# Performance work log

Measured on AMD Instinct MI355X. Metric: run time of the kernel, lower is better.

## Reference

```python
import jax, jax.numpy as jnp
import numpy as np
from jax import lax

B, C, XH, XW, KH, KW = 32, 128, 96, 96, 3, 3
BN_EPS = 1e-5


def setup_inputs() -> dict:
    key = jax.random.key(0)
    k1, k2, k3 = jax.random.split(key, 3)
    x = jax.random.normal(k1, (B, C, XH, XW), dtype=jnp.float32)
    k = jax.random.normal(k2, (B, C, KH, KW), dtype=jnp.float32)
    pw_weight = jax.random.normal(k3, (C, C), dtype=jnp.float32) * (1.0 / np.sqrt(C))
    bn_gamma = jnp.ones((C,), dtype=jnp.float32)
    bn_beta = jnp.zeros((C,), dtype=jnp.float32)
    bn_mean = jnp.zeros((C,), dtype=jnp.float32)
    bn_var = jnp.ones((C,), dtype=jnp.float32)
    return {"x": x, "k": k, "pw_weight": pw_weight, "bn_gamma": bn_gamma,
            "bn_beta": bn_beta, "bn_mean": bn_mean, "bn_var": bn_var}


def _depthwise_one(xi, ki):
    # xi: [C, XH, XW], ki: [C, KH, KW] -> per-sample depthwise conv, padding=KH//2
    pad = KH // 2
    out = lax.conv_general_dilated(
        xi[None],                 # [1, C, XH, XW]
        ki[:, None],              # [C, 1, KH, KW]  (OIHW with groups=C)
        window_strides=(1, 1),
        padding=((pad, pad), (pad, pad)),
        feature_group_count=C,
        dimension_numbers=("NCHW", "OIHW", "NCHW"),
    )
    return out[0]


def reference(x, k, pw_weight, bn_gamma, bn_beta, bn_mean, bn_var):
    # Per-sample dynamic depthwise conv, batched via vmap (replaces the Python loop)
    x_new = jax.vmap(_depthwise_one)(x, k)          # [B, C, XH, XW]
    # 1x1 pointwise conv (no bias)
    y = jnp.einsum("bchw,oc->bohw", x_new, pw_weight)
    # BatchNorm (inference form with running stats) + ReLU
    inv = bn_gamma * lax.rsqrt(bn_var + BN_EPS)
    y = y * inv[None, :, None, None] + (bn_beta - bn_mean * inv)[None, :, None, None]
    return jax.nn.relu(y)
```

## Files before the change

### kernel.cpp

```cpp
#include <hip/hip_runtime.h>
#include <hip/hip_bf16.h>

#define BB 32
#define CC 128
#define HH 96
#define WW 96
#define BN_EPS 1e-5f

typedef __attribute__((ext_vector_type(8))) short bf16x8_t;
typedef __attribute__((ext_vector_type(4))) float f32x4_t;
typedef __attribute__((ext_vector_type(4), aligned(4))) float f32x4u_t;
typedef __attribute__((ext_vector_type(2))) unsigned int u32x2_t;
typedef __attribute__((ext_vector_type(4))) unsigned int u32x4_t;

__global__ __launch_bounds__(256)
void prep_kernel(const float* __restrict__ pw,
                 const float* __restrict__ g, const float* __restrict__ b,
                 const float* __restrict__ m, const float* __restrict__ v,
                 unsigned short* __restrict__ wper,
                 float* __restrict__ inv, float* __restrict__ bias)
{
    int t = blockIdx.x * 256 + threadIdx.x;
    if (t < CC * CC) {
        int o = t >> 7, cidx = t & 127;
        int kc = cidx >> 5, r = cidx & 31, gg = r >> 3, j = r & 7;
        int c = kc * 32 + gg * 4 + (j & 3) + 16 * (j >> 2);
        __hip_bfloat16 h = __float2bfloat16(pw[o * CC + c]);
        wper[o * CC + cidx] = *reinterpret_cast<unsigned short*>(&h);
    }
    if (t < CC) {
        float iv = g[t] * rsqrtf(v[t] + BN_EPS);
        inv[t] = iv;
        bias[t] = b[t] - m[t] * iv;
    }
}

__global__ __launch_bounds__(256, 6)
void dw_kernel(const float* __restrict__ x, const float* __restrict__ kk,
               unsigned short* __restrict__ xn)
{
    const unsigned wg  = blockIdx.x;
    const unsigned bid = (wg & 7u) * 2304u + (wg >> 3);
    const int u = (int)bid * 256 + threadIdx.x;
    const int lane = threadIdx.x & 63;
    const int woct = u % 12;
    int t1 = u / 12;
    const int h = t1 % HH;
    int t2 = t1 / HH;
    const int cs = t2 & 127;
    const int b  = t2 >> 7;

    const int kc = cs >> 5, rr = cs & 31, gg = rr >> 3, jj = rr & 7;
    const int c = kc * 32 + gg * 4 + (jj & 3) + 16 * (jj >> 2);

    const int w0 = woct * 8;
    const bool l_edge = (woct == 0);
    const bool r_edge = (woct == 11);

    const float* plane = x + (size_t)(b * CC + c) * (HH * WW);

    float kw[9];
    {
        const float* kp = kk + (size_t)(b * CC + c) * 9;
        f32x4u_t q0 = *(const f32x4u_t*)(kp);
        f32x4u_t q1 = *(const f32x4u_t*)(kp + 4);
        kw[0]=q0.x; kw[1]=q0.y; kw[2]=q0.z; kw[3]=q0.w;
        kw[4]=q1.x; kw[5]=q1.y; kw[6]=q1.z; kw[7]=q1.w;
        kw[8]=kp[8];
    }

    float r0[10], r1[10], r2[10];
    auto load_row = [&](int row, float* o) {
        const bool valid = (row >= 0) && (row < HH);
        const int rrow = row < 0 ? 0 : (row >= HH ? HH - 1 : row);
        const float* rp = plane + rrow * WW + w0;
        f32x4_t M0 = *(const f32x4_t*)rp;
        f32x4_t M1 = *(const f32x4_t*)(rp + 4);
        float vl = __shfl_up(M1.w, 1);
        float vr = __shfl_down(M0.x, 1);
        if (lane == 0  && !l_edge) vl = rp[-1];
        if (lane == 63 && !r_edge) vr = rp[8];
        o[0] = (valid && !l_edge) ? vl : 0.f;
        o[1] = valid ? M0.x : 0.f;
        o[2] = valid ? M0.y : 0.f;
        o[3] = valid ? M0.z : 0.f;
        o[4] = valid ? M0.w : 0.f;
        o[5] = valid ? M1.x : 0.f;
        o[6] = valid ? M1.y : 0.f;
        o[7] = valid ? M1.z : 0.f;
        o[8] = valid ? M1.w : 0.f;
        o[9] = (valid && !r_edge) ? vr : 0.f;
    };

    load_row(h - 1, r0);
    load_row(h,     r1);
    load_row(h + 1, r2);

    unsigned pkw[4];
    #pragma unroll
    for (int i = 0; i < 4; ++i) {
        float s0 = 0.f, s1 = 0.f;
        #pragma unroll
        for (int t = 0; t < 3; ++t) {
            s0 = fmaf(r0[2 * i + t],     kw[t],     s0);
            s0 = fmaf(r1[2 * i + t],     kw[3 + t], s0);
            s0 = fmaf(r2[2 * i + t],     kw[6 + t], s0);
            s1 = fmaf(r0[2 * i + 1 + t], kw[t],     s1);
            s1 = fmaf(r1[2 * i + 1 + t], kw[3 + t], s1);
            s1 = fmaf(r2[2 * i + 1 + t], kw[6 + t], s1);
        }
        __hip_bfloat16 h0b = __float2bfloat16(s0);
        __hip_bfloat16 h1b = __float2bfloat16(s1);
        pkw[i] = (unsigned)*reinterpret_cast<unsigned short*>(&h0b)
               | ((unsigned)*reinterpret_cast<unsigned short*>(&h1b) << 16);
    }
    u32x4_t pk;
    pk.x = pkw[0]; pk.y = pkw[1]; pk.z = pkw[2]; pk.w = pkw[3];
    unsigned short* dst = xn + ((size_t)(b * CC + cs) * (HH * WW) + (size_t)h * WW + w0);
    *reinterpret_cast<u32x4_t*>(dst) = pk;
}

__global__ __launch_bounds__(256, 3)
void pw_kernel(const unsigned short* __restrict__ xn,
               const unsigned short* __restrict__ wper,
               const float* __restrict__ invp, const float* __restrict__ biasp,
               float* __restrict__ out)
{
    __shared__ __align__(16) unsigned char xnb[128 * 256];
    const int tid = threadIdx.x;

    const unsigned wg  = blockIdx.x;
    const unsigned nid = (wg & 7u) * 96u + (wg >> 3);
    const int tw  = nid % 6u;
    const int thg = (nid / 6u) % 4u;
    const int b   = nid / 24u;
    const int w0  = tw * 16;

    const int lane   = tid & 63;
    const int wv     = tid >> 6;
    const int lo     = lane & 15;
    const int hi     = lane >> 4;
    const int o_base = wv * 32;

    bf16x8_t wfrag[2][4];
    #pragma unroll
    for (int t2 = 0; t2 < 2; ++t2)
        #pragma unroll
        for (int kc = 0; kc < 4; ++kc)
            wfrag[t2][kc] = *reinterpret_cast<const bf16x8_t*>(
                wper + (size_t)(o_base + t2 * 16 + lo) * CC + kc * 32 + hi * 8);

    float iv2[2], bs2[2];
    #pragma unroll
    for (int t2 = 0; t2 < 2; ++t2) {
        iv2[t2] = invp[o_base + t2 * 16 + lo];
        bs2[t2] = biasp[o_base + t2 * 16 + lo];
    }

    const int cs4 = tid >> 3;
    const int py  = tid & 7;
    const unsigned short* src_base =
        xn + (size_t)(b * CC + cs4 * 4) * (HH * WW) + (size_t)py * WW + w0;

    unsigned dLA[4][4], dRA[4][4], dLB[4][4], dRB[4][4];

    auto LOADREGS = [&](int t, unsigned (*dL)[4], unsigned (*dR)[4]) {
        const unsigned short* s0 = src_base + (size_t)((thg * 3 + t) * 8) * WW;
        #pragma unroll
        for (int q = 0; q < 4; ++q) {
            const unsigned short* src = s0 + (size_t)q * (HH * WW);
            u32x4_t L = *(const u32x4_t*)src;
            u32x4_t R = *(const u32x4_t*)(src + 8);
            dL[q][0]=L.x; dL[q][1]=L.y; dL[q][2]=L.z; dL[q][3]=L.w;
            dR[q][0]=R.x; dR[q][1]=R.y; dR[q][2]=R.z; dR[q][3]=R.w;
        }
    };

    auto WRITE_LDS = [&](unsigned (*dL)[4], unsigned (*dR)[4]) {
        #pragma unroll
        for (int o8 = 0; o8 < 2; ++o8) {
            #pragma unroll
            for (int j = 0; j < 4; ++j) {
                const unsigned d0 = o8 ? dR[0][j] : dL[0][j];
                const unsigned d1 = o8 ? dR[1][j] : dL[1][j];
                const unsigned d2 = o8 ? dR[2][j] : dL[2][j];
                const unsigned d3 = o8 ? dR[3][j] : dL[3][j];
                u32x2_t we, wo;
                we.x = __builtin_amdgcn_perm(d1, d0, 0x05040100u);
                we.y = __builtin_amdgcn_perm(d3, d2, 0x05040100u);
                wo.x = __builtin_amdgcn_perm(d1, d0, 0x07060302u);
                wo.y = __builtin_amdgcn_perm(d3, d2, 0x07060302u);
                const int pe = py * 16 + o8 * 8 + 2 * j;
                const int po = pe + 1;
                *reinterpret_cast<u32x2_t*>(&xnb[(unsigned)pe * 256 +
                    (((unsigned)cs4 * 8) ^ (((unsigned)pe & 7u) << 4))]) = we;
                *reinterpret_cast<u32x2_t*>(&xnb[(unsigned)po * 256 +
                    (((unsigned)cs4 * 8) ^ (((unsigned)po & 7u) << 4))]) = wo;
            }
        }
    };

    auto COMPUTE = [&](int t) {
        const int h0 = (thg * 3 + t) * 8;
        f32x4_t acc[8][2];
        #pragma unroll
        for (int pt = 0; pt < 8; ++pt) {
            acc[pt][0] = (f32x4_t){0.f, 0.f, 0.f, 0.f};
            acc[pt][1] = (f32x4_t){0.f, 0.f, 0.f, 0.f};
        }
        #pragma unroll
        for (int pt = 0; pt < 8; ++pt) {
            const unsigned rowbase = (unsigned)(pt * 16 + lo) * 256;
            const unsigned sw = (unsigned)((lo & 7) << 4);
            #pragma unroll
            for (int kc = 0; kc < 4; ++kc) {
                bf16x8_t xfrag = *reinterpret_cast<const bf16x8_t*>(
                    &xnb[rowbase + (((unsigned)(kc * 64 + hi * 16)) ^ sw)]);
                acc[pt][0] = __builtin_amdgcn_mfma_f32_16x16x32_bf16(
                    xfrag, wfrag[0][kc], acc[pt][0], 0, 0, 0);
                acc[pt][1] = __builtin_amdgcn_mfma_f32_16x16x32_bf16(
                    xfrag, wfrag[1][kc], acc[pt][1], 0, 0, 0);
            }
        }
        #pragma unroll
        for (int pt = 0; pt < 8; ++pt) {
            const int hrow = h0 + pt;
            #pragma unroll
            for (int t2 = 0; t2 < 2; ++t2) {
                const int o = o_base + t2 * 16 + lo;
                f32x4_t vv;
                #pragma unroll
                for (int r = 0; r < 4; ++r)
                    vv[r] = fmaxf(fmaf(acc[pt][t2][r], iv2[t2], bs2[t2]), 0.f);
                __builtin_nontemporal_store(vv, reinterpret_cast<f32x4_t*>(
                    out + ((size_t)(b * CC + o) * HH + hrow) * WW + w0 + hi * 4));
            }
        }
    };

    LOADREGS(0, dLA, dRA);
    WRITE_LDS(dLA, dRA);
    LOADREGS(1, dLB, dRB);
    __syncthreads();
    COMPUTE(0);
    __syncthreads();
    WRITE_LDS(dLB, dRB);
    LOADREGS(2, dLA, dRA);
    __syncthreads();
    COMPUTE(1);
    __syncthreads();
    WRITE_LDS(dLA, dRA);
    __syncthreads();
    COMPUTE(2);
}

__global__ __launch_bounds__(256, 3)
void fused_main(const float* __restrict__ x, const float* __restrict__ kk,
                const unsigned short* __restrict__ wper,
                const float* __restrict__ invp, const float* __restrict__ biasp,
                float* __restrict__ out)
{
    __shared__ __align__(16) unsigned char xnb[128 * 256];
    const int tid = threadIdx.x;
    const unsigned wg  = blockIdx.x;
    const unsigned nid = (wg & 7u) * 288u + (wg >> 3);
    const int bx = nid % 6u;
    const int by = (nid / 6u) % 12u;
    const int bb = nid / 72u;
    const int w0 = bx * 16;
    const int h0 = by * 8;
    {
        const int wq = tid & 3;
        const int cp = tid >> 2;
        const int s  = cp << 1;
        const int kc = s >> 5, rr = s & 31, gg = rr >> 3, jj = rr & 7;
        const int cA = kc * 32 + gg * 4 + (jj & 3) + 16 * (jj >> 2);
        const int gw = w0 + wq * 4;
        const bool l_edge = (gw == 0);
        const bool r_edge = (gw + 4 >= WW);
        const float* planeA = x + (size_t)(bb * CC + cA) * (HH * WW);
        float kwA[9], kwB[9];
        {
            const float* kp = kk + (size_t)(bb * CC + cA) * 9;
            f32x4u_t q0 = *(const f32x4u_t*)(kp + 0);
            f32x4u_t q1 = *(const f32x4u_t*)(kp + 4);
            f32x4u_t q2 = *(const f32x4u_t*)(kp + 8);
            f32x4u_t q3 = *(const f32x4u_t*)(kp + 12);
            float     e16 = kp[16], e17 = kp[17];
            kwA[0]=q0.x; kwA[1]=q0.y; kwA[2]=q0.z; kwA[3]=q0.w;
            kwA[4]=q1.x; kwA[5]=q1.y; kwA[6]=q1.z; kwA[7]=q1.w;
            kwA[8]=q2.x;
            kwB[0]=q2.y; kwB[1]=q2.z; kwB[2]=q2.w;
            kwB[3]=q3.x; kwB[4]=q3.y; kwB[5]=q3.z; kwB[6]=q3.w;
            kwB[7]=e16;  kwB[8]=e17;
        }
        float xd[2][10][6];
        #pragma unroll
        for (int q = 0; q < 2; ++q) {
            const float* plane = planeA + q * (HH * WW);
            #pragma unroll
            for (int r = 0; r < 10; ++r) {
                const int row = h0 - 1 + r;
                const bool valid = (row >= 0) && (row < HH);
                const int rrow = row < 0 ? 0 : (row >= HH ? HH - 1 : row);
                const float* rp = plane + rrow * WW + gw;
                f32x4_t M = *(const f32x4_t*)rp;
                float vl = rp[l_edge ? 0 : -1];
                float vr = rp[r_edge ? 3 : 4];
                xd[q][r][0] = (valid && !l_edge) ? vl : 0.f;
                xd[q][r][1] = valid ? M.x : 0.f;
                xd[q][r][2] = valid ? M.y : 0.f;
                xd[q][r][3] = valid ? M.z : 0.f;
                xd[q][r][4] = valid ? M.w : 0.f;
                xd[q][r][5] = (valid && !r_edge) ? vr : 0.f;
            }
        }
        #pragma unroll
        for (int py = 0; py < 8; ++py) {
            #pragma unroll
            for (int i = 0; i < 4; ++i) {
                float sA = 0.f, sB = 0.f;
                #pragma unroll
                for (int t = 0; t < 3; ++t) {
                    sA = fmaf(xd[0][py + 0][i + t], kwA[t],     sA);
                    sA = fmaf(xd[0][py + 1][i + t], kwA[3 + t], sA);
                    sA = fmaf(xd[0][py + 2][i + t], kwA[6 + t], sA);
                    sB = fmaf(xd[1][py + 0][i + t], kwB[t],     sB);
                    sB = fmaf(xd[1][py + 1][i + t], kwB[3 + t], sB);
                    sB = fmaf(xd[1][py + 2][i + t], kwB[6 + t], sB);
                }
                __hip_bfloat16 hA = __float2bfloat16(sA);
                __hip_bfloat16 hB = __float2bfloat16(sB);
                unsigned pk = (unsigned)*reinterpret_cast<unsigned short*>(&hA)
                            | ((unsigned)*reinterpret_cast<unsigned short*>(&hB) << 16);
                const int p = py * 16 + wq * 4 + i;
                const unsigned boff = ((unsigned)(cp << 2)) ^ (((unsigned)p & 7u) << 4);
                *reinterpret_cast<unsigned*>(&xnb[(unsigned)p * 256 + boff]) = pk;
            }
        }
    }
    __syncthreads();
    {
        const int lane   = tid & 63;
        const int wv     = tid >> 6;
        const int lo     = lane & 15;
        const int hi     = lane >> 4;
        const int o_base = wv * 32;
        bf16x8_t afrag[2][4];
        #pragma unroll
        for (int t2 = 0; t2 < 2; ++t2)
            #pragma unroll
            for (int kc = 0; kc < 4; ++kc)
                afrag[t2][kc] = *reinterpret_cast<const bf16x8_t*>(
                    wper + (size_t)(o_base + t2 * 16 + lo) * CC + kc * 32 + hi * 8);
        f32x4_t acc[8][2];
        #pragma unroll
        for (int pt = 0; pt < 8; ++pt) {
            acc[pt][0] = (f32x4_t){0.f, 0.f, 0.f, 0.f};
            acc[pt][1] = (f32x4_t){0.f, 0.f, 0.f, 0.f};
        }
        #pragma unroll
        for (int pt = 0; pt < 8; ++pt) {
            const unsigned rowbase = (unsigned)(pt * 16 + lo) * 256;
            const unsigned sw = (unsigned)((lo & 7) << 4);
            #pragma unroll
            for (int kc = 0; kc < 4; ++kc) {
                bf16x8_t bfrag = *reinterpret_cast<const bf16x8_t*>(
                    &xnb[rowbase + (((unsigned)(kc * 64 + hi * 16)) ^ sw)]);
                acc[pt][0] = __builtin_amdgcn_mfma_f32_16x16x32_bf16(
                    afrag[0][kc], bfrag, acc[pt][0], 0, 0, 0);
                acc[pt][1] = __builtin_amdgcn_mfma_f32_16x16x32_bf16(
                    afrag[1][kc], bfrag, acc[pt][1], 0, 0, 0);
            }
        }
        float iv[2][4], bs[2][4];
        #pragma unroll
        for (int t2 = 0; t2 < 2; ++t2)
            #pragma unroll
            for (int r = 0; r < 4; ++r) {
                const int o = o_base + t2 * 16 + hi * 4 + r;
                iv[t2][r] = invp[o];
                bs[t2][r] = biasp[o];
            }
        #pragma unroll
        for (int pt = 0; pt < 8; ++pt) {
            const int hrow = h0 + pt;
            #pragma unroll
            for (int t2 = 0; t2 < 2; ++t2) {
                #pragma unroll
                for (int r = 0; r < 4; ++r) {
                    const int o = o_base + t2 * 16 + hi * 4 + r;
                    float val = fmaf(acc[pt][t2][r], iv[t2][r], bs[t2][r]);
                    val = fmaxf(val, 0.f);
                    out[((size_t)(bb * CC + o) * HH + hrow) * WW + w0 + lo] = val;
                }
            }
        }
    }
}

extern "C" void kernel_launch(void* const* d_in, const int* in_sizes, int n_in,
                              void* d_out, int out_size, void* d_ws, size_t ws_size,
                              hipStream_t stream) {
    const float* x   = (const float*)d_in[0];
    const float* kk  = (const float*)d_in[1];
    const float* pwt = (const float*)d_in[2];
    const float* g   = (const float*)d_in[3];
    const float* b   = (const float*)d_in[4];
    const float* m   = (const float*)d_in[5];
    const float* v   = (const float*)d_in[6];
    float* out = (float*)d_out;

    unsigned short* wper = (unsigned short*)d_ws;
    float* inv  = (float*)((char*)d_ws + 32768);
    float* bias = (float*)((char*)d_ws + 32768 + 512);
    unsigned short* xn = (unsigned short*)((char*)d_ws + 36864);
    const size_t need = 36864 + (size_t)BB * CC * HH * WW * 2;

    prep_kernel<<<64, 256, 0, stream>>>(pwt, g, b, m, v, wper, inv, bias);
    if (ws_size >= need) {
        dw_kernel<<<dim3(18432), 256, 0, stream>>>(x, kk, xn);
        pw_kernel<<<dim3(768), 256, 0, stream>>>(xn, wper, inv, bias, out);
    } else {
        fused_main<<<dim3(2304), 256, 0, stream>>>(x, kk, wper, inv, bias, out);
    }
}
```

Before: 98.84 us.

## Stage depthwise input rows in LDS tiles per 16-row slab

The depthwise kernel now gives each workgroup a 16-row slab of one channel plane. It loads 18 rows (including halos) into shared memory with vectorized loads, and each thread computes 6 outputs from LDS. This replaces the per-thread 3-row global loads and cross-lane shuffles, which read each input row three times. The cost is an extra barrier, narrower 4-byte output stores, and more workgroups in the grid.

```diff
diff --git a/kernel.cpp b/kernel.cpp
--- a/kernel.cpp
+++ b/kernel.cpp
@@ -39,85 +39,90 @@
 void dw_kernel(const float* __restrict__ x, const float* __restrict__ kk,
                unsigned short* __restrict__ xn)
 {
+    __shared__ float tile[18 * 96];
+    const int tid = threadIdx.x;
+
     const unsigned wg  = blockIdx.x;
-    const unsigned bid = (wg & 7u) * 2304u + (wg >> 3);
-    const int u = (int)bid * 256 + threadIdx.x;
-    const int lane = threadIdx.x & 63;
-    const int woct = u % 12;
-    int t1 = u / 12;
-    const int h = t1 % HH;
-    int t2 = t1 / HH;
-    const int cs = t2 & 127;
-    const int b  = t2 >> 7;
+    const unsigned bid = (wg & 7u) * 3072u + (wg >> 3);
+    const int slab = bid % 6u;
+    const int cs   = (bid / 6u) % 128u;
+    const int b    = bid / 768u;
+    const int h0   = slab * 16;
 
     const int kc = cs >> 5, rr = cs & 31, gg = rr >> 3, jj = rr & 7;
     const int c = kc * 32 + gg * 4 + (jj & 3) + 16 * (jj >> 2);
 
-    const int w0 = woct * 8;
-    const bool l_edge = (woct == 0);
-    const bool r_edge = (woct == 11);
-
     const float* plane = x + (size_t)(b * CC + c) * (HH * WW);
 
-    float kw[9];
-    {
-        const float* kp = kk + (size_t)(b * CC + c) * 9;
-        f32x4u_t q0 = *(const f32x4u_t*)(kp);
-        f32x4u_t q1 = *(const f32x4u_t*)(kp + 4);
-        kw[0]=q0.x; kw[1]=q0.y; kw[2]=q0.z; kw[3]=q0.w;
-        kw[4]=q1.x; kw[5]=q1.y; kw[6]=q1.z; kw[7]=q1.w;
-        kw[8]=kp[8];
-    }
-
-    float r0[10], r1[10], r2[10];
-    auto load_row = [&](int row, float* o) {
-        const bool valid = (row >= 0) && (row < HH);
-        const int rrow = row < 0 ? 0 : (row >= HH ? HH - 1 : row);
-        const float* rp = plane + rrow * WW + w0;
-        f32x4_t M0 = *(const f32x4_t*)rp;
-        f32x4_t M1 = *(const f32x4_t*)(rp + 4);
-        float vl = __shfl_up(M1.w, 1);
-        float vr = __shfl_down(M0.x, 1);
-        if (lane == 0  && !l_edge) vl = rp[-1];
-        if (lane == 63 && !r_edge) vr = rp[8];
-        o[0] = (valid && !l_edge) ? vl : 0.f;
-        o[1] = valid ? M0.x : 0.f;
-        o[2] = valid ? M0.y : 0.f;
-        o[3] = valid ? M0.z : 0.f;
-        o[4] = valid ? M0.w : 0.f;
-        o[5] = valid ? M1.x : 0.f;
-        o[6] = valid ? M1.y : 0.f;
-        o[7] = valid ? M1.z : 0.f;
-        o[8] = valid ? M1.w : 0.f;
-        o[9] = (valid && !r_edge) ? vr : 0.f;
-    };
-
-    load_row(h - 1, r0);
-    load_row(h,     r1);
-    load_row(h + 1, r2);
-
-    unsigned pkw[4];
+    const float* kp = kk + (size_t)(b * CC + c) * 9;
+    const float kw0 = kp[0], kw1 = kp[1], kw2 = kp[2];
+    const float kw3 = kp[3], kw4 = kp[4], kw5 = kp[5];
+    const float kw6 = kp[6], kw7 = kp[7], kw8 = kp[8];
+
     #pragma unroll
-    for (int i = 0; i < 4; ++i) {
-        float s0 = 0.f, s1 = 0.f;
-        #pragma unroll
-        for (int t = 0; t < 3; ++t) {
-            s0 = fmaf(r0[2 * i + t],     kw[t],     s0);
-            s0 = fmaf(r1[2 * i + t],     kw[3 + t], s0);
-            s0 = fmaf(r2[2 * i + t],     kw[6 + t], s0);
-            s1 = fmaf(r0[2 * i + 1 + t], kw[t],     s1);
-            s1 = fmaf(r1[2 * i + 1 + t], kw[3 + t], s1);
-            s1 = fmaf(r2[2 * i + 1 + t], kw[6 + t], s1);
-        }
+    for (int it = 0; it < 2; ++it) {
+        const int s = tid + it * 256;
+        if (s < 432) {
+            const int row  = s / 24;
+            const int col4 = (s % 24) * 4;
+            const int hh   = h0 - 1 + row;
+            f32x4_t val = (f32x4_t){0.f, 0.f, 0.f, 0.f};
+            if (hh >= 0 && hh < HH)
+                val = *(const f32x4_t*)(plane + (size_t)hh * WW + col4);
+            *(f32x4_t*)&tile[row * 96 + col4] = val;
+        }
+    }
+    __syncthreads();
+
+    const int r  = tid >> 4;
+    const int cc = (tid & 15) * 6;
+
+    float v[3][8];
+    #pragma unroll
+    for (int dr = 0; dr < 3; ++dr) {
+        const float* trow = &tile[(r + dr) * 96];
+        const float lv = trow[cc == 0 ? 0 : cc - 1];
+        v[dr][0] = (cc == 0) ? 0.f : lv;
+        #pragma unroll
+        for (int i = 0; i < 6; ++i) v[dr][1 + i] = trow[cc + i];
+        const float rv = trow[cc == 90 ? 95 : cc + 6];
+        v[dr][7] = (cc == 90) ? 0.f : rv;
+    }
+
+    unsigned pk[3];
+    #pragma unroll
+    for (int pr = 0; pr < 3; ++pr) {
+        float s0, s1;
+        const int j0 = 2 * pr;
+        s0 = v[0][j0] * kw0;                   const int j1 = j0 + 1;
+        s0 = fmaf(v[0][j0 + 1], kw1, s0);
+        s0 = fmaf(v[0][j0 + 2], kw2, s0);
+        s0 = fmaf(v[1][j0],     kw3, s0);
+        s0 = fmaf(v[1][j0 + 1], kw4, s0);
+        s0 = fmaf(v[1][j0 + 2], kw5, s0);
+        s0 = fmaf(v[2][j0],     kw6, s0);
+        s0 = fmaf(v[2][j0 + 1], kw7, s0);
+        s0 = fmaf(v[2][j0 + 2], kw8, s0);
+        s1 = v[0][j1] * kw0;
+        s1 = fmaf(v[0][j1 + 1], kw1, s1);
+        s1 = fmaf(v[0][j1 + 2], kw2, s1);
+        s1 = fmaf(v[1][j1],     kw3, s1);
+        s1 = fmaf(v[1][j1 + 1], kw4, s1);
+        s1 = fmaf(v[1][j1 + 2], kw5, s1);
+        s1 = fmaf(v[2][j1],     kw6, s1);
+        s1 = fmaf(v[2][j1 + 1], kw7, s1);
+        s1 = fmaf(v[2][j1 + 2], kw8, s1);
         __hip_bfloat16 h0b = __float2bfloat16(s0);
         __hip_bfloat16 h1b = __float2bfloat16(s1);
-        pkw[i] = (unsigned)*reinterpret_cast<unsigned short*>(&h0b)
+        pk[pr] = (unsigned)*reinterpret_cast<unsigned short*>(&h0b)
                | ((unsigned)*reinterpret_cast<unsigned short*>(&h1b) << 16);
     }
-    u32x4_t pk;
-    pk.x = pkw[0]; pk.y = pkw[1]; pk.z = pkw[2]; pk.w = pkw[3];
-    unsigned short* dst = xn + ((size_t)(b * CC + cs) * (HH * WW) + (size_t)h * WW + w0);
-    *reinterpret_cast<u32x4_t*>(dst) = pk;
+
+    unsigned short* dst = xn + (size_t)(b * CC + cs) * (HH * WW)
+                             + (size_t)(h0 + r) * WW + cc;
+    *reinterpret_cast<unsigned*>(dst)     = pk[0];
+    *reinterpret_cast<unsigned*>(dst + 2) = pk[1];
+    *reinterpret_cast<unsigned*>(dst + 4) = pk[2];
 }
 
 __global__ __launch_bounds__(256, 3)
@@ -230,8 +235,8 @@
                 const int o = o_base + t2 * 16 + lo;
                 f32x4_t vv;
                 #pragma unroll
-                for (int r = 0; r < 4; ++r)
-                    vv[r] = fmaxf(fmaf(acc[pt][t2][r], iv2[t2], bs2[t2]), 0.f);
+                for (int rix = 0; rix < 4; ++rix)
+                    vv[rix] = fmaxf(fmaf(acc[pt][t2][rix], iv2[t2], bs2[t2]), 0.f);
                 __builtin_nontemporal_store(vv, reinterpret_cast<f32x4_t*>(
                     out + ((size_t)(b * CC + o) * HH + hrow) * WW + w0 + hi * 4));
             }
@@ -419,7 +424,7 @@
 
     prep_kernel<<<64, 256, 0, stream>>>(pwt, g, b, m, v, wper, inv, bias);
     if (ws_size >= need) {
-        dw_kernel<<<dim3(18432), 256, 0, stream>>>(x, kk, xn);
+        dw_kernel<<<dim3(24576), 256, 0, stream>>>(x, kk, xn);
         pw_kernel<<<dim3(768), 256, 0, stream>>>(xn, wper, inv, bias, out);
     } else {
         fused_main<<<dim3(2304), 256, 0, stream>>>(x, kk, wper, inv, bias, out);
```

Measured after the change: 94.49 us. -4.4%, faster.
